# Performance work log

Hardware: AMD Instinct MI355X
Metric: run time of the kernel (lower is better)

Reference implementation:

```python
import jax, jax.numpy as jnp
import numpy as np
from jax import lax

SEQ, FEAT, U1, U2, U3, OUT = 20, 5, 10, 7, 4, 4
BATCH = 262144


def _he_uniform(key, shape, fan_in):
    lim = np.sqrt(6.0 / fan_in)
    return jax.random.uniform(key, shape, jnp.float32, -lim, lim)


def _orthogonal(key, n, m):
    a = jax.random.normal(key, (max(n, m), min(n, m)), jnp.float32)
    q, _ = jnp.linalg.qr(a)
    return q[:n, :m] if n >= m else q[:m, :n].T


def _lstm_params(key, in_dim, units):
    k1, k2 = jax.random.split(key)
    Wk = _he_uniform(k1, (in_dim, 4 * units), in_dim)
    Wr = _orthogonal(k2, units, 4 * units)
    # Keras unit_forget_bias: bias = [zeros(i), ones(f), zeros(c), zeros(o)]
    b = jnp.concatenate([jnp.zeros(units), jnp.ones(units), jnp.zeros(2 * units)]).astype(jnp.float32)
    return Wk, Wr, b


def setup_inputs() -> dict:
    key = jax.random.key(0)
    ks = jax.random.split(key, 5)
    x = jax.random.normal(ks[0], (BATCH, SEQ, FEAT), jnp.float32)
    Wk1, Wr1, b1 = _lstm_params(ks[1], FEAT, U1)
    Wk2, Wr2, b2 = _lstm_params(ks[2], U1, U2)
    Wk3, Wr3, b3 = _lstm_params(ks[3], U2, U3)
    kd1, kd2 = jax.random.split(ks[4])
    lim = np.sqrt(6.0 / (U3 + OUT))  # glorot_uniform (Dense default)
    Wd = jax.random.uniform(kd1, (U3, OUT), jnp.float32, -lim, lim)
    bd = jnp.zeros((OUT,), jnp.float32)
    return {"x": x, "Wk1": Wk1, "Wr1": Wr1, "b1": b1,
            "Wk2": Wk2, "Wr2": Wr2, "b2": b2,
            "Wk3": Wk3, "Wr3": Wr3, "b3": b3,
            "Wd": Wd, "bd": bd}


def lstm_layer(x, Wk, Wr, b):
    # x: [B, T, F] -> h-sequence [B, T, U]; Keras gate order i, f, c(g), o
    B = x.shape[0]
    U = Wr.shape[0]
    # precompute input projection for all timesteps (one big GEMM)
    zx = jnp.einsum('btf,fg->btg', x, Wk) + b  # [B, T, 4U]
    zxT = jnp.swapaxes(zx, 0, 1)               # [T, B, 4U]

    def step(carry, zt):
        h, c = carry
        z = zt + h @ Wr
        i, f, g, o = jnp.split(z, 4, axis=-1)
        i = jax.nn.sigmoid(i)
        f = jax.nn.sigmoid(f)
        g = jnp.tanh(g)
        o = jax.nn.sigmoid(o)
        c = f * c + i * g
        h = o * jnp.tanh(c)
        return (h, c), h

    init = (jnp.zeros((B, U), x.dtype), jnp.zeros((B, U), x.dtype))
    _, hs = lax.scan(step, init, zxT)
    return jnp.swapaxes(hs, 0, 1)  # [B, T, U]


def reference(x, Wk1, Wr1, b1, Wk2, Wr2, b2, Wk3, Wr3, b3, Wd, bd):
    h = lstm_layer(x, Wk1, Wr1, b1)
    h = lstm_layer(h, Wk2, Wr2, b2)
    h = lstm_layer(h, Wk3, Wr3, b3)
    return jax.nn.sigmoid(jnp.einsum('btu,uo->bto', h, Wd) + bd)
```

## Files before the change

kernel.cpp:

```cpp
#include <hip/hip_runtime.h>

static constexpr int SEQ = 20, FEAT = 5, NU1 = 10, NU2 = 7, NU3 = 4, NOUT = 4;

typedef short bf16x8 __attribute__((ext_vector_type(8)));
typedef float f32x4  __attribute__((ext_vector_type(4)));


__device__ __forceinline__ unsigned short bf16_hi_rne(float x) {
    unsigned u = __float_as_uint(x);
    return (unsigned short)((u + 0x7FFF + ((u >> 16) & 1)) >> 16);
}
__device__ __forceinline__ unsigned short bf16_trunc(float x) {
    return (unsigned short)(__float_as_uint(x) >> 16);
}
__device__ __forceinline__ float bf16_to_f(unsigned short h) {
    return __uint_as_float(((unsigned)h) << 16);
}
__device__ __forceinline__ unsigned hpack(float h) {
    unsigned rp;
    asm("v_cvt_pk_bf16_f32 %0, %1, %1" : "=v"(rp) : "v"(h));
    float lo = h - __uint_as_float(rp << 16);
    return __builtin_amdgcn_perm(__float_as_uint(lo), rp, 0x07060100u);
}

__device__ __forceinline__ float sigm(float x) {
    return __builtin_amdgcn_rcpf(1.0f + __builtin_amdgcn_exp2f(x * -1.4426950408889634f));
}
__device__ __forceinline__ float ftanh(float x) {
    return 1.0f - 2.0f * __builtin_amdgcn_rcpf(1.0f + __builtin_amdgcn_exp2f(x * 2.8853900817779268f));
}

__device__ __forceinline__ unsigned act_unit(const f32x4 z, float& c) {
    float gi = sigm(z[0]), gf = sigm(z[1]), gg = ftanh(z[2]), go = sigm(z[3]);
    c = gf * c + gi * gg;
    return hpack(go * ftanh(c));
}

__device__ __forceinline__ unsigned bperm(int idx, unsigned v) {
    return (unsigned)__builtin_amdgcn_ds_bpermute(idx, (int)v);
}
__device__ __forceinline__ bf16x8 bfrag(unsigned v0, unsigned v1) {
    uint4 u{v0, v0, v1, v1};
    return __builtin_bit_cast(bf16x8, u);
}

__global__ void build_afrags(const float* Wk1, const float* Wr1, const float* b1,
                             const float* Wk2, const float* Wr2, const float* b2,
                             const float* Wk3, const float* Wr3, const float* b3,
                             const float* Wd,  const float* bd, unsigned* ws) {
    const int lane = threadIdx.x;
    const int m = lane & 15;
    const int qh = lane >> 4;

    for (int tau = 0; tau < 3; ++tau)
    for (int kap = 0; kap < 2; ++kap) {
        unsigned short h8[8];
        for (int j = 0; j < 8; ++j) {
            const int k = kap * 32 + qh * 8 + j;
            const int i = k >> 2, cls = k & 3;
            const int u = tau * 4 + (m >> 2), col = (m & 3) * NU1 + u;
            unsigned short v = 0;
            if (u < NU1) {
                if (i < 15) {
                    float W;
                    if (i < 8)       W = Wr1[((i >> 1) + 4 * (i & 1)) * 40 + col];
                    else if (i < 10) W = Wr1[i * 40 + col];
                    else             W = Wk1[(i - 10) * 40 + col];
                    unsigned short hi = bf16_hi_rne(W);
                    v = (cls < 2) ? hi : bf16_trunc(W - bf16_to_f(hi));
                } else if (i == 15) {
                    float bv = b1[col];
                    unsigned short hi = bf16_hi_rne(bv);
                    v = (cls == 0) ? hi : ((cls == 1) ? bf16_trunc(bv - bf16_to_f(hi)) : (unsigned short)0);
                }
            }
            h8[j] = v;
        }
        const int id = tau * 2 + kap;
        for (int d = 0; d < 4; ++d)
            ws[id * 256 + lane * 4 + d] = (unsigned)h8[2 * d] | ((unsigned)h8[2 * d + 1] << 16);
    }
    for (int tau = 0; tau < 2; ++tau)
    for (int kap = 0; kap < 3; ++kap) {
        unsigned short h8[8];
        for (int j = 0; j < 8; ++j) {
            const int k = kap * 32 + qh * 8 + j;
            const int i = k >> 2, cls = k & 3;
            const int u = tau * 4 + (m >> 2), col = (m & 3) * NU2 + u;
            unsigned short v = 0;
            if (u < NU2) {
                if (i < 17) {
                    float W;
                    if (i < 8)        W = Wk2[((i >> 1) + 4 * (i & 1)) * 28 + col];
                    else if (i < 10)  W = Wk2[i * 28 + col];
                    else if (i < 16)  W = Wr2[(((i - 10) >> 1) + 4 * ((i - 10) & 1)) * 28 + col];
                    else              W = Wr2[3 * 28 + col];
                    unsigned short hi = bf16_hi_rne(W);
                    v = (cls < 2) ? hi : bf16_trunc(W - bf16_to_f(hi));
                } else if (i == 17) {
                    float bv = b2[col];
                    unsigned short hi = bf16_hi_rne(bv);
                    v = (cls == 0) ? hi : ((cls == 1) ? bf16_trunc(bv - bf16_to_f(hi)) : (unsigned short)0);
                }
            }
            h8[j] = v;
        }
        const int id = 6 + tau * 3 + kap;
        for (int d = 0; d < 4; ++d)
            ws[id * 256 + lane * 4 + d] = (unsigned)h8[2 * d] | ((unsigned)h8[2 * d + 1] << 16);
    }
    for (int kap = 0; kap < 2; ++kap) {
        unsigned short h8[8];
        for (int j = 0; j < 8; ++j) {
            const int k = kap * 32 + qh * 8 + j;
            const int i = k >> 2, cls = k & 3;
            const int u = m >> 2, col = (m & 3) * NU3 + u;
            unsigned short v = 0;
            if (i < 11) {
                float W;
                if (i < 6)       W = Wk3[((i >> 1) + 4 * (i & 1)) * 16 + col];
                else if (i == 6) W = Wk3[3 * 16 + col];
                else             W = Wr3[(i - 7) * 16 + col];
                unsigned short hi = bf16_hi_rne(W);
                v = (cls < 2) ? hi : bf16_trunc(W - bf16_to_f(hi));
            } else if (i == 11) {
                float bv = b3[col];
                unsigned short hi = bf16_hi_rne(bv);
                v = (cls == 0) ? hi : ((cls == 1) ? bf16_trunc(bv - bf16_to_f(hi)) : (unsigned short)0);
            }
            h8[j] = v;
        }
        const int id = 12 + kap;
        for (int d = 0; d < 4; ++d)
            ws[id * 256 + lane * 4 + d] = (unsigned)h8[2 * d] | ((unsigned)h8[2 * d + 1] << 16);
    }
    {
        unsigned short h8[8];
        for (int j = 0; j < 8; ++j) {
            const int k = qh * 8 + j;
            const int i = k >> 2, cls = k & 3;
            unsigned short v = 0;
            if (m < NOUT) {
                if (i < 4) {
                    float W = Wd[i * NOUT + m];
                    unsigned short hi = bf16_hi_rne(W);
                    v = (cls < 2) ? hi : bf16_trunc(W - bf16_to_f(hi));
                } else if (i == 4) {
                    float bv = bd[m];
                    unsigned short hi = bf16_hi_rne(bv);
                    v = (cls == 0) ? hi : ((cls == 1) ? bf16_trunc(bv - bf16_to_f(hi)) : (unsigned short)0);
                }
            }
            h8[j] = v;
        }
        for (int d = 0; d < 4; ++d)
            ws[14 * 256 + lane * 4 + d] = (unsigned)h8[2 * d] | ((unsigned)h8[2 * d + 1] << 16);
    }
}

__global__ __launch_bounds__(256, 4) void lstm3_mfma(
    const float* __restrict__ x, const unsigned* __restrict__ wsA,
    float* __restrict__ out, int B) {
    const int tid = threadIdx.x;
    const int lane = tid & 63;
    const int n = lane & 15;
    const int q = lane >> 4;

    bf16x8 af[15];
#pragma unroll
    for (int i = 0; i < 15; ++i) {
        uint4 v = ((const uint4*)wsA)[i * 64 + lane];
        af[i] = __builtin_bit_cast(bf16x8, v);
    }

    const int i_h19 = (n + 16) << 2;
    const int i_sh  = (n + 16 * ((q + 3) & 3)) << 2;
    const int i_r1  = (n + 16 * ((q + 1) & 3)) << 2;
    const int i_r2  = (n + 16 * ((q + 2) & 3)) << 2;

    const unsigned ONE = 0x3F803F80u;
    const f32x4 zro = {0.f, 0.f, 0.f, 0.f};

    const int ngrp = B >> 4;
    const int gw = (blockIdx.x * blockDim.x + tid) >> 6;
    const int nw = (gridDim.x * blockDim.x) >> 6;

    for (int grp = gw; grp < ngrp; grp += nw) {
        const float* xr = x + (size_t)grp * 16 * (SEQ * FEAT) + n * (SEQ * FEAT);
        float* ob = out + (size_t)grp * 16 * (SEQ * NOUT) + n * (SEQ * NOUT);

        unsigned p1a = 0, p1b = 0, p1c = 0, t9 = 0;
        unsigned p2a = 0, p2b = 0, p3 = 0, rot = 0, rot2 = 0;
        float c10 = 0.f, c11 = 0.f, c12 = 0.f, c20 = 0.f, c21 = 0.f, c30 = 0.f;

        float xa = 0.f, xc = 0.f;
        if (q != 0) {
            const float* p = xr + 2 * (q - 1);
            xa = p[0];
            if (q != 3) xc = p[1];
        }

#pragma unroll 1
        for (int t = 0; t < SEQ; ++t) {
            const unsigned xP0 = hpack(xa), xP1 = hpack(xc);
            {
                const int tn = (t + 1 < SEQ) ? t + 1 : 0;
                if (q != 0) {
                    const float* p = xr + tn * FEAT + 2 * (q - 1);
                    xa = p[0];
                    if (q != 3) xc = p[1];
                }
            }
            bf16x8 bF0 = bfrag(p1a, p1b);
            unsigned F1v0 = (q == 0) ? p1c : xP0;
            unsigned F1v1 = (q == 0) ? t9 : ((q == 3) ? ONE : xP1);
            bf16x8 bF1 = bfrag(F1v0, F1v1);
            f32x4 z0 = __builtin_amdgcn_mfma_f32_16x16x32_bf16(af[0], bF0, zro, 0, 0, 0);
            z0 = __builtin_amdgcn_mfma_f32_16x16x32_bf16(af[1], bF1, z0, 0, 0, 0);
            f32x4 z1 = __builtin_amdgcn_mfma_f32_16x16x32_bf16(af[2], bF0, zro, 0, 0, 0);
            z1 = __builtin_amdgcn_mfma_f32_16x16x32_bf16(af[3], bF1, z1, 0, 0, 0);
            f32x4 z2 = __builtin_amdgcn_mfma_f32_16x16x32_bf16(af[4], bF0, zro, 0, 0, 0);
            z2 = __builtin_amdgcn_mfma_f32_16x16x32_bf16(af[5], bF1, z2, 0, 0, 0);
            const unsigned s2a = bperm(i_sh, p2a);
            const unsigned s2b = bperm(i_sh, p2b);
            p1a = act_unit(z0, c10);
            p1b = act_unit(z1, c11);
            p1c = act_unit(z2, c12);
            t9  = bperm(i_h19, p1c);
            bf16x8 bA  = bfrag(p1a, p1b);
            unsigned F2v0 = (q == 0) ? p1c : s2a;
            unsigned F2v1 = (q == 0) ? t9  : s2b;
            bf16x8 bF2 = bfrag(F2v0, F2v1);
            bf16x8 bF3 = bfrag(s2a, ONE);
            f32x4 y0 = __builtin_amdgcn_mfma_f32_16x16x32_bf16(af[6], bA, zro, 0, 0, 0);
            y0 = __builtin_amdgcn_mfma_f32_16x16x32_bf16(af[7], bF2, y0, 0, 0, 0);
            y0 = __builtin_amdgcn_mfma_f32_16x16x32_bf16(af[8], bF3, y0, 0, 0, 0);
            f32x4 y1 = __builtin_amdgcn_mfma_f32_16x16x32_bf16(af[9], bA, zro, 0, 0, 0);
            y1 = __builtin_amdgcn_mfma_f32_16x16x32_bf16(af[10], bF2, y1, 0, 0, 0);
            y1 = __builtin_amdgcn_mfma_f32_16x16x32_bf16(af[11], bF3, y1, 0, 0, 0);
            p2a = act_unit(y0, c20);
            p2b = act_unit(y1, c21);
            bf16x8 bF4 = bfrag(p2a, (q == 3) ? rot : p2b);
            unsigned F5v0 = (q == 0) ? rot  : rot2;
            unsigned F5v1 = (q == 0) ? rot2 : ONE;
            bf16x8 bF5 = bfrag(F5v0, F5v1);
            f32x4 w0 = __builtin_amdgcn_mfma_f32_16x16x32_bf16(af[12], bF4, zro, 0, 0, 0);
            w0 = __builtin_amdgcn_mfma_f32_16x16x32_bf16(af[13], bF5, w0, 0, 0, 0);
            p3 = act_unit(w0, c30);
            rot  = bperm(i_r1, p3);
            rot2 = bperm(i_r2, p3);
            unsigned F6v0 = (q == 0) ? p3 : ((q == 1) ? rot : ONE);
            unsigned F6v1 = (q == 0) ? rot : rot2;
            f32x4 o0 = __builtin_amdgcn_mfma_f32_16x16x32_bf16(af[14], bfrag(F6v0, F6v1), zro, 0, 0, 0);
            if (q == 0) {
                float4 o4;
                o4.x = sigm(o0[0]); o4.y = sigm(o0[1]);
                o4.z = sigm(o0[2]); o4.w = sigm(o0[3]);
                *(float4*)(ob + t * NOUT) = o4;
            }
        }
    }
}

extern "C" void kernel_launch(void* const* d_in, const int* in_sizes, int n_in,
                              void* d_out, int out_size, void* d_ws, size_t ws_size,
                              hipStream_t stream) {
    const float* x   = (const float*)d_in[0];
    const float* Wk1 = (const float*)d_in[1];
    const float* Wr1 = (const float*)d_in[2];
    const float* b1  = (const float*)d_in[3];
    const float* Wk2 = (const float*)d_in[4];
    const float* Wr2 = (const float*)d_in[5];
    const float* b2  = (const float*)d_in[6];
    const float* Wk3 = (const float*)d_in[7];
    const float* Wr3 = (const float*)d_in[8];
    const float* b3  = (const float*)d_in[9];
    const float* Wd  = (const float*)d_in[10];
    const float* bd  = (const float*)d_in[11];
    float* out = (float*)d_out;
    unsigned* ws = (unsigned*)d_ws;

    const int B = in_sizes[0] / (SEQ * FEAT);

    build_afrags<<<1, 64, 0, stream>>>(Wk1, Wr1, b1, Wk2, Wr2, b2,
                                       Wk3, Wr3, b3, Wd, bd, ws);
    lstm3_mfma<<<2048, 256, 0, stream>>>(x, ws, out, B);
}
```

Before: 386.2 us.

## Interleave two independent batch groups per wave and spread output sigmoid across lanes

Result: faster. 376.0 us (-2.6%).

```diff
diff --git a/kernel.cpp b/kernel.cpp
--- a/kernel.cpp
+++ b/kernel.cpp
@@ -4,6 +4,8 @@
 
 typedef short bf16x8 __attribute__((ext_vector_type(8)));
 typedef float f32x4  __attribute__((ext_vector_type(4)));
+
+static constexpr unsigned ONE_P = 0x3F803F80u;
 
 
 __device__ __forceinline__ unsigned short bf16_hi_rne(float x) {
@@ -42,6 +44,9 @@
 __device__ __forceinline__ bf16x8 bfrag(unsigned v0, unsigned v1) {
     uint4 u{v0, v0, v1, v1};
     return __builtin_bit_cast(bf16x8, u);
+}
+__device__ __forceinline__ f32x4 MF(bf16x8 a, bf16x8 b, f32x4 c) {
+    return __builtin_amdgcn_mfma_f32_16x16x32_bf16(a, b, c, 0, 0, 0);
 }
 
 __global__ void build_afrags(const float* Wk1, const float* Wr1, const float* b1,
@@ -140,16 +145,14 @@
             const int k = qh * 8 + j;
             const int i = k >> 2, cls = k & 3;
             unsigned short v = 0;
-            if (m < NOUT) {
-                if (i < 4) {
-                    float W = Wd[i * NOUT + m];
-                    unsigned short hi = bf16_hi_rne(W);
-                    v = (cls < 2) ? hi : bf16_trunc(W - bf16_to_f(hi));
-                } else if (i == 4) {
-                    float bv = bd[m];
-                    unsigned short hi = bf16_hi_rne(bv);
-                    v = (cls == 0) ? hi : ((cls == 1) ? bf16_trunc(bv - bf16_to_f(hi)) : (unsigned short)0);
-                }
+            if (i < 4) {
+                float W = Wd[i * NOUT + (m & 3)];
+                unsigned short hi = bf16_hi_rne(W);
+                v = (cls < 2) ? hi : bf16_trunc(W - bf16_to_f(hi));
+            } else if (i == 4) {
+                float bv = bd[m & 3];
+                unsigned short hi = bf16_hi_rne(bv);
+                v = (cls == 0) ? hi : ((cls == 1) ? bf16_trunc(bv - bf16_to_f(hi)) : (unsigned short)0);
             }
             h8[j] = v;
         }
@@ -158,7 +161,152 @@
     }
 }
 
-__global__ __launch_bounds__(256, 4) void lstm3_mfma(
+struct Ctx {
+    bf16x8 af[15];
+    int i_h19, i_sh, i_r1, i_r2;
+    int q;
+};
+
+struct Chain {
+    const float* xr;
+    float* ob;
+    unsigned p1a, p1b, p1c, t9, p2a, p2b, p3, rot, rot2;
+    unsigned s2a, s2b, xP0, xP1;
+    float c10, c11, c12, c20, c21, c30;
+    float xa, xc;
+    float d0, d1, d2, d3;
+    f32x4 z0, z1, z2, y0, y1, w0;
+};
+
+__device__ __forceinline__ void ph_init(Chain& S, const float* x, float* out,
+                                        int grp, int n, int q) {
+    S.xr = x + (size_t)grp * 16 * (SEQ * FEAT) + n * (SEQ * FEAT);
+    S.ob = out + (size_t)grp * 16 * (SEQ * NOUT) + n * (SEQ * NOUT);
+    S.p1a = S.p1b = S.p1c = S.t9 = S.p2a = S.p2b = S.p3 = S.rot = S.rot2 = 0;
+    S.c10 = S.c11 = S.c12 = S.c20 = S.c21 = S.c30 = 0.f;
+    S.xa = S.xc = 0.f;
+    S.d0 = S.d1 = S.d2 = S.d3 = 0.f;
+    if (q != 0) {
+        const float* p = S.xr + 2 * (q - 1);
+        S.xa = p[0];
+        if (q != 3) S.xc = p[1];
+    }
+}
+
+__device__ __forceinline__ void ph_pre(Chain& S, int t, int q) {
+    S.xP0 = hpack(S.xa);
+    S.xP1 = hpack(S.xc);
+    const int tn = (t + 1 < SEQ) ? t + 1 : 0;
+    if (q != 0) {
+        const float* p = S.xr + tn * FEAT + 2 * (q - 1);
+        S.xa = p[0];
+        if (q != 3) S.xc = p[1];
+    }
+}
+
+__device__ __forceinline__ void ph_L1(Chain& S, const Ctx& C) {
+    const f32x4 zro = {0.f, 0.f, 0.f, 0.f};
+    bf16x8 bF0 = bfrag(S.p1a, S.p1b);
+    unsigned F1v0 = (C.q == 0) ? S.p1c : S.xP0;
+    unsigned F1v1 = (C.q == 0) ? S.t9 : ((C.q == 3) ? ONE_P : S.xP1);
+    bf16x8 bF1 = bfrag(F1v0, F1v1);
+    S.z0 = MF(C.af[0], bF0, zro); S.z0 = MF(C.af[1], bF1, S.z0);
+    S.z1 = MF(C.af[2], bF0, zro); S.z1 = MF(C.af[3], bF1, S.z1);
+    S.z2 = MF(C.af[4], bF0, zro); S.z2 = MF(C.af[5], bF1, S.z2);
+    S.s2a = bperm(C.i_sh, S.p2a);
+    S.s2b = bperm(C.i_sh, S.p2b);
+}
+
+__device__ __forceinline__ void ph_act1(Chain& S, const Ctx& C) {
+    S.p1a = act_unit(S.z0, S.c10);
+    S.p1b = act_unit(S.z1, S.c11);
+    S.p1c = act_unit(S.z2, S.c12);
+    S.t9  = bperm(C.i_h19, S.p1c);
+}
+
+__device__ __forceinline__ void ph_L2(Chain& S, const Ctx& C) {
+    const f32x4 zro = {0.f, 0.f, 0.f, 0.f};
+    bf16x8 bA = bfrag(S.p1a, S.p1b);
+    unsigned F2v0 = (C.q == 0) ? S.p1c : S.s2a;
+    unsigned F2v1 = (C.q == 0) ? S.t9  : S.s2b;
+    bf16x8 bF2 = bfrag(F2v0, F2v1);
+    bf16x8 bF3 = bfrag(S.s2a, ONE_P);
+    S.y0 = MF(C.af[6], bA, zro);
+    S.y0 = MF(C.af[7], bF2, S.y0);
+    S.y0 = MF(C.af[8], bF3, S.y0);
+    S.y1 = MF(C.af[9], bA, zro);
+    S.y1 = MF(C.af[10], bF2, S.y1);
+    S.y1 = MF(C.af[11], bF3, S.y1);
+}
+
+__device__ __forceinline__ void ph_act2(Chain& S) {
+    S.p2a = act_unit(S.y0, S.c20);
+    S.p2b = act_unit(S.y1, S.c21);
+}
+
+__device__ __forceinline__ void ph_L3(Chain& S, const Ctx& C) {
+    const f32x4 zro = {0.f, 0.f, 0.f, 0.f};
+    bf16x8 bF4 = bfrag(S.p2a, (C.q == 3) ? S.rot : S.p2b);
+    unsigned F5v0 = (C.q == 0) ? S.rot  : S.rot2;
+    unsigned F5v1 = (C.q == 0) ? S.rot2 : ONE_P;
+    bf16x8 bF5 = bfrag(F5v0, F5v1);
+    S.w0 = MF(C.af[12], bF4, zro);
+    S.w0 = MF(C.af[13], bF5, S.w0);
+}
+
+__device__ __forceinline__ void ph_act3(Chain& S, const Ctx& C) {
+    S.p3 = act_unit(S.w0, S.c30);
+    S.rot  = bperm(C.i_r1, S.p3);
+    S.rot2 = bperm(C.i_r2, S.p3);
+}
+
+__device__ __forceinline__ void ph_D(Chain& S, const Ctx& C, int t) {
+    const f32x4 zro = {0.f, 0.f, 0.f, 0.f};
+    unsigned F6v0 = (C.q == 0) ? S.p3 : ((C.q == 1) ? S.rot : ONE_P);
+    unsigned F6v1 = (C.q == 0) ? S.rot : S.rot2;
+    f32x4 o0 = MF(C.af[14], bfrag(F6v0, F6v1), zro);
+    float v01 = (C.q & 1) ? o0[1] : o0[0];
+    float v23 = (C.q & 1) ? o0[3] : o0[2];
+    float v = (C.q & 2) ? v23 : v01;
+    const int r = t & 3;
+    S.d0 = (r == 0) ? v : S.d0;
+    S.d1 = (r == 1) ? v : S.d1;
+    S.d2 = (r == 2) ? v : S.d2;
+    S.d3 = (r == 3) ? v : S.d3;
+}
+
+__device__ __forceinline__ void ph_flush(Chain& S, int t, int q) {
+    float* p = S.ob + (t - 3) * NOUT + q;
+    p[0 * NOUT] = sigm(S.d0);
+    p[1 * NOUT] = sigm(S.d1);
+    p[2 * NOUT] = sigm(S.d2);
+    p[3 * NOUT] = sigm(S.d3);
+}
+
+template <bool DUAL>
+__device__ __forceinline__ void run_groups(const Ctx& C, const float* x, float* out,
+                                           int g0, int g1, int n, int q) {
+    Chain S0, S1;
+    ph_init(S0, x, out, g0, n, q);
+    if constexpr (DUAL) ph_init(S1, x, out, g1, n, q);
+#pragma unroll 1
+    for (int t = 0; t < SEQ; ++t) {
+        ph_pre(S0, t, q);   if constexpr (DUAL) ph_pre(S1, t, q);
+        ph_L1(S0, C);       if constexpr (DUAL) ph_L1(S1, C);
+        ph_act1(S0, C);     if constexpr (DUAL) ph_act1(S1, C);
+        ph_L2(S0, C);       if constexpr (DUAL) ph_L2(S1, C);
+        ph_act2(S0);        if constexpr (DUAL) ph_act2(S1);
+        ph_L3(S0, C);       if constexpr (DUAL) ph_L3(S1, C);
+        ph_act3(S0, C);     if constexpr (DUAL) ph_act3(S1, C);
+        ph_D(S0, C, t);     if constexpr (DUAL) ph_D(S1, C, t);
+        if ((t & 3) == 3) {
+            ph_flush(S0, t, q);
+            if constexpr (DUAL) ph_flush(S1, t, q);
+        }
+    }
+}
+
+__global__ __launch_bounds__(256, 3) void lstm3_mfma(
     const float* __restrict__ x, const unsigned* __restrict__ wsA,
     float* __restrict__ out, int B) {
     const int tid = threadIdx.x;
@@ -166,99 +314,28 @@
     const int n = lane & 15;
     const int q = lane >> 4;
 
-    bf16x8 af[15];
+    Ctx C;
 #pragma unroll
     for (int i = 0; i < 15; ++i) {
         uint4 v = ((const uint4*)wsA)[i * 64 + lane];
-        af[i] = __builtin_bit_cast(bf16x8, v);
-    }
-
-    const int i_h19 = (n + 16) << 2;
-    const int i_sh  = (n + 16 * ((q + 3) & 3)) << 2;
-    const int i_r1  = (n + 16 * ((q + 1) & 3)) << 2;
-    const int i_r2  = (n + 16 * ((q + 2) & 3)) << 2;
-
-    const unsigned ONE = 0x3F803F80u;
-    const f32x4 zro = {0.f, 0.f, 0.f, 0.f};
+        C.af[i] = __builtin_bit_cast(bf16x8, v);
+    }
+    C.i_h19 = (n + 16) << 2;
+    C.i_sh  = (n + 16 * ((q + 3) & 3)) << 2;
+    C.i_r1  = (n + 16 * ((q + 1) & 3)) << 2;
+    C.i_r2  = (n + 16 * ((q + 2) & 3)) << 2;
+    C.q = q;
 
     const int ngrp = B >> 4;
     const int gw = (blockIdx.x * blockDim.x + tid) >> 6;
     const int nw = (gridDim.x * blockDim.x) >> 6;
 
-    for (int grp = gw; grp < ngrp; grp += nw) {
-        const float* xr = x + (size_t)grp * 16 * (SEQ * FEAT) + n * (SEQ * FEAT);
-        float* ob = out + (size_t)grp * 16 * (SEQ * NOUT) + n * (SEQ * NOUT);
-
-        unsigned p1a = 0, p1b = 0, p1c = 0, t9 = 0;
-        unsigned p2a = 0, p2b = 0, p3 = 0, rot = 0, rot2 = 0;
-        float c10 = 0.f, c11 = 0.f, c12 = 0.f, c20 = 0.f, c21 = 0.f, c30 = 0.f;
-
-        float xa = 0.f, xc = 0.f;
-        if (q != 0) {
-            const float* p = xr + 2 * (q - 1);
-            xa = p[0];
-            if (q != 3) xc = p[1];
-        }
-
-#pragma unroll 1
-        for (int t = 0; t < SEQ; ++t) {
-            const unsigned xP0 = hpack(xa), xP1 = hpack(xc);
-            {
-                const int tn = (t + 1 < SEQ) ? t + 1 : 0;
-                if (q != 0) {
-                    const float* p = xr + tn * FEAT + 2 * (q - 1);
-                    xa = p[0];
-                    if (q != 3) xc = p[1];
-                }
-            }
-            bf16x8 bF0 = bfrag(p1a, p1b);
-            unsigned F1v0 = (q == 0) ? p1c : xP0;
-            unsigned F1v1 = (q == 0) ? t9 : ((q == 3) ? ONE : xP1);
-            bf16x8 bF1 = bfrag(F1v0, F1v1);
-            f32x4 z0 = __builtin_amdgcn_mfma_f32_16x16x32_bf16(af[0], bF0, zro, 0, 0, 0);
-            z0 = __builtin_amdgcn_mfma_f32_16x16x32_bf16(af[1], bF1, z0, 0, 0, 0);
-            f32x4 z1 = __builtin_amdgcn_mfma_f32_16x16x32_bf16(af[2], bF0, zro, 0, 0, 0);
-            z1 = __builtin_amdgcn_mfma_f32_16x16x32_bf16(af[3], bF1, z1, 0, 0, 0);
-            f32x4 z2 = __builtin_amdgcn_mfma_f32_16x16x32_bf16(af[4], bF0, zro, 0, 0, 0);
-            z2 = __builtin_amdgcn_mfma_f32_16x16x32_bf16(af[5], bF1, z2, 0, 0, 0);
-            const unsigned s2a = bperm(i_sh, p2a);
-            const unsigned s2b = bperm(i_sh, p2b);
-            p1a = act_unit(z0, c10);
-            p1b = act_unit(z1, c11);
-            p1c = act_unit(z2, c12);
-            t9  = bperm(i_h19, p1c);
-            bf16x8 bA  = bfrag(p1a, p1b);
-            unsigned F2v0 = (q == 0) ? p1c : s2a;
-            unsigned F2v1 = (q == 0) ? t9  : s2b;
-            bf16x8 bF2 = bfrag(F2v0, F2v1);
-            bf16x8 bF3 = bfrag(s2a, ONE);
-            f32x4 y0 = __builtin_amdgcn_mfma_f32_16x16x32_bf16(af[6], bA, zro, 0, 0, 0);
-            y0 = __builtin_amdgcn_mfma_f32_16x16x32_bf16(af[7], bF2, y0, 0, 0, 0);
-            y0 = __builtin_amdgcn_mfma_f32_16x16x32_bf16(af[8], bF3, y0, 0, 0, 0);
-            f32x4 y1 = __builtin_amdgcn_mfma_f32_16x16x32_bf16(af[9], bA, zro, 0, 0, 0);
-            y1 = __builtin_amdgcn_mfma_f32_16x16x32_bf16(af[10], bF2, y1, 0, 0, 0);
-            y1 = __builtin_amdgcn_mfma_f32_16x16x32_bf16(af[11], bF3, y1, 0, 0, 0);
-            p2a = act_unit(y0, c20);
-            p2b = act_unit(y1, c21);
-            bf16x8 bF4 = bfrag(p2a, (q == 3) ? rot : p2b);
-            unsigned F5v0 = (q == 0) ? rot  : rot2;
-            unsigned F5v1 = (q == 0) ? rot2 : ONE;
-            bf16x8 bF5 = bfrag(F5v0, F5v1);
-            f32x4 w0 = __builtin_amdgcn_mfma_f32_16x16x32_bf16(af[12], bF4, zro, 0, 0, 0);
-            w0 = __builtin_amdgcn_mfma_f32_16x16x32_bf16(af[13], bF5, w0, 0, 0, 0);
-            p3 = act_unit(w0, c30);
-            rot  = bperm(i_r1, p3);
-            rot2 = bperm(i_r2, p3);
-            unsigned F6v0 = (q == 0) ? p3 : ((q == 1) ? rot : ONE);
-            unsigned F6v1 = (q == 0) ? rot : rot2;
-            f32x4 o0 = __builtin_amdgcn_mfma_f32_16x16x32_bf16(af[14], bfrag(F6v0, F6v1), zro, 0, 0, 0);
-            if (q == 0) {
-                float4 o4;
-                o4.x = sigm(o0[0]); o4.y = sigm(o0[1]);
-                o4.z = sigm(o0[2]); o4.w = sigm(o0[3]);
-                *(float4*)(ob + t * NOUT) = o4;
-            }
-        }
+    for (int g0 = 2 * gw; g0 < ngrp; g0 += 2 * nw) {
+        const int g1 = g0 + 1;
+        if (g1 < ngrp)
+            run_groups<true>(C, x, out, g0, g1, n, q);
+        else
+            run_groups<false>(C, x, out, g0, g0, n, q);
     }
 }
 
```
